# Kernel optimization log

Hardware: AMD Instinct MI355X
Metric: run time of the kernel (lower is better)

Reference implementation:

```python
import jax, jax.numpy as jnp
import numpy as np

N_NODES = 100_000
N_EDGES = 1_600_000
D = 128
BN_EPS = 1e-5
GIN_EPS = 0.0  # GINConv default eps, train_eps=False


def setup_inputs() -> dict:
    key = jax.random.key(0)
    ks = jax.random.split(key, 8)
    x = jax.random.normal(ks[0], (N_NODES, D), dtype=jnp.float32)
    edge_index = jax.random.randint(ks[1], (2, N_EDGES), 0, N_NODES, dtype=jnp.int64)
    s = 1.0 / np.sqrt(D)
    W1 = jax.random.uniform(ks[2], (D, D), jnp.float32, -s, s)
    b1 = jax.random.uniform(ks[3], (D,), jnp.float32, -s, s)
    W2 = jax.random.uniform(ks[4], (D, D), jnp.float32, -s, s)
    b2 = jax.random.uniform(ks[5], (D,), jnp.float32, -s, s)
    W3 = jax.random.uniform(ks[6], (D, D), jnp.float32, -s, s)
    g1 = jnp.ones((D,), jnp.float32)
    be1 = jnp.zeros((D,), jnp.float32)
    g2 = jnp.ones((D,), jnp.float32)
    be2 = jnp.zeros((D,), jnp.float32)
    return {"x": x, "edge_index": edge_index,
            "W1": W1, "b1": b1, "g1": g1, "be1": be1,
            "W2": W2, "b2": b2, "g2": g2, "be2": be2,
            "W3": W3}


def _batchnorm(h, gamma, beta):
    # training-mode BatchNorm1d over node dim with biased variance
    mean = jnp.mean(h, axis=0)
    var = jnp.mean(jnp.square(h - mean), axis=0)
    return (h - mean) * jax.lax.rsqrt(var + BN_EPS) * gamma + beta


def reference(x, edge_index, W1, b1, g1, be1, W2, b2, g2, be2, W3):
    src, dst = edge_index[0], edge_index[1]
    # GIN aggregation: (1+eps)*x_i + sum_{j->i} x_j  (scatter-add over edges)
    agg = jax.ops.segment_sum(x[src], dst, num_segments=N_NODES)
    h = (1.0 + GIN_EPS) * x + agg
    # MLP: Linear+BN+ReLU x2, then Linear (no bias)
    h = jax.nn.relu(_batchnorm(h @ W1.T + b1, g1, be1))
    h = jax.nn.relu(_batchnorm(h @ W2.T + b2, g2, be2))
    h = h @ W3.T
    # GINLayer final activation (bn=None)
    return jax.nn.relu(h)
```

## Files before the change

kernel.cpp:

```cpp
#include <hip/hip_runtime.h>

#define NN 100000
#define NE 1600000
#define DD 128
#define NCB 782
#define TILE 2048
#define NTILE 782
#define SREP 16
#define WPAD 17408

typedef __attribute__((ext_vector_type(8))) short bf16x8;
typedef __attribute__((ext_vector_type(4))) float f32x4;

union u4bf8 { uint4 u; bf16x8 v; };

__device__ __forceinline__ ushort f2bf(float f) {
    union { float f; uint i; } v; v.f = f;
    uint i = v.i;
    return (ushort)((i + 0x7fffu + ((i >> 16) & 1u)) >> 16);
}
__device__ __forceinline__ float bf2f(ushort u) {
    union { uint i; float f; } v; v.i = ((uint)u) << 16; return v.f;
}
__device__ __forceinline__ float blo(uint v) { return bf2f((ushort)(v & 0xffffu)); }
__device__ __forceinline__ float bhi(uint v) { return bf2f((ushort)(v >> 16)); }

__global__ __launch_bounds__(256) void k_xbh(const float* __restrict__ x,
                                             uint* __restrict__ xb,
                                             const int* __restrict__ ei,
                                             int* __restrict__ ghistP,
                                             const float* __restrict__ W1,
                                             const float* __restrict__ W2,
                                             const float* __restrict__ W3,
                                             ushort* __restrict__ Wbp) {
    __shared__ int h[NCB];
    int t = threadIdx.x;
    for (int i = t; i < NCB; i += 256) h[i] = 0;
    __syncthreads();
    int base = blockIdx.x * TILE;
#pragma unroll
    for (int i = 0; i < 8; ++i) {
        int e = base + i * 256 + t;
        if (e < NE) atomicAdd(&h[ei[NE + e] >> 7], 1);
    }
    int gid = blockIdx.x * 256 + t;
#pragma unroll
    for (int i = 0; i < 8; ++i) {
        int item = i * (NTILE * 256) + gid;
        if (item < NN * 16) {
            int n = item >> 4, q = item & 15;
            const float* xp = x + (size_t)n * DD + q * 8;
            float4 a = *(const float4*)xp;
            float4 b = *(const float4*)(xp + 4);
            uint4 pk;
            pk.x = (uint)f2bf(a.x) | ((uint)f2bf(a.y) << 16);
            pk.y = (uint)f2bf(a.z) | ((uint)f2bf(a.w) << 16);
            pk.z = (uint)f2bf(b.x) | ((uint)f2bf(b.y) << 16);
            pk.w = (uint)f2bf(b.z) | ((uint)f2bf(b.w) << 16);
            *(uint4*)(xb + (size_t)n * 64 + q * 4) = pk;
        }
    }
    int c = gid;
    if (c < 6144) {
        int l = c >> 11;
        int cc = c & 2047;
        int r = cc >> 4, c8 = (cc & 15) * 8;
        const float* Wl = (l == 0) ? W1 : (l == 1) ? W2 : W3;
        const float* p = Wl + r * DD + c8;
        float4 a = *(const float4*)p;
        float4 b = *(const float4*)(p + 4);
        uint4 pk;
        pk.x = (uint)f2bf(a.x) | ((uint)f2bf(a.y) << 16);
        pk.y = (uint)f2bf(a.z) | ((uint)f2bf(a.w) << 16);
        pk.z = (uint)f2bf(b.x) | ((uint)f2bf(b.y) << 16);
        pk.w = (uint)f2bf(b.z) | ((uint)f2bf(b.w) << 16);
        *(uint4*)&Wbp[(size_t)l * WPAD + r * 136 + c8] = pk;
    }
    __syncthreads();
    for (int i = t; i < NCB; i += 256)
        if (h[i] > 0) atomicAdd(&ghistP[i * 16], h[i]);
}

__global__ void k_cscan(const int* __restrict__ ghistP, int* __restrict__ cb,
                        int* __restrict__ gcurP) {
    __shared__ int sh[1024];
    int t = threadIdx.x;
    int my = (t < NCB) ? ghistP[t * 16] : 0;
    sh[t] = my;
    __syncthreads();
    for (int o = 1; o < 1024; o <<= 1) {
        int u = (t >= o) ? sh[t - o] : 0;
        __syncthreads();
        sh[t] += u;
        __syncthreads();
    }
    if (t < NCB) { int ex = sh[t] - my; cb[t] = ex; gcurP[t * 16] = ex; }
    if (t == NCB - 1) cb[NCB] = sh[t];
}

__global__ __launch_bounds__(256) void k_cscatter(const int* __restrict__ ei,
                                                  int* __restrict__ gcurP,
                                                  uint* __restrict__ buck) {
    __shared__ int h[NCB];
    __shared__ int tb[NCB];
    int t = threadIdx.x;
    for (int i = t; i < NCB; i += 256) h[i] = 0;
    __syncthreads();
    int base = blockIdx.x * TILE;
    uint vv[8]; int bb[8], rr[8];
#pragma unroll
    for (int i = 0; i < 8; ++i) {
        int e = base + i * 256 + t;
        bb[i] = -1;
        if (e < NE) {
            int s = ei[e], d = ei[NE + e];
            int b = d >> 7;
            bb[i] = b;
            vv[i] = (uint)s | ((uint)(d & 127) << 17);
            rr[i] = atomicAdd(&h[b], 1);
        }
    }
    __syncthreads();
    for (int i = t; i < NCB; i += 256)
        if (h[i] > 0) tb[i] = atomicAdd(&gcurP[i * 16], h[i]);
    __syncthreads();
#pragma unroll
    for (int i = 0; i < 8; ++i) {
        if (bb[i] >= 0) buck[tb[bb[i]] + rr[i]] = vv[i];
    }
}

__global__ __launch_bounds__(256) void k_fsort(const uint* __restrict__ buck,
                                               const int* __restrict__ cb,
                                               int* __restrict__ csr,
                                               int* __restrict__ rowp) {
    __shared__ int cnt[128];
    __shared__ int sd[64];
    int c = blockIdx.x, t = threadIdx.x;
    if (t < 128) cnt[t] = 0;
    __syncthreads();
    int s0 = cb[c], s1 = cb[c + 1];
    for (int i = s0 + t; i < s1; i += 256)
        atomicAdd(&cnt[(buck[i] >> 17) & 127], 1);
    __syncthreads();
    int p = 0, q = 0;
    if (t < 64) { p = cnt[2 * t]; q = cnt[2 * t + 1]; sd[t] = p + q; }
    __syncthreads();
    for (int o = 1; o < 64; o <<= 1) {
        int u = (t >= o && t < 64) ? sd[t - o] : 0;
        __syncthreads();
        if (t < 64) sd[t] += u;
        __syncthreads();
    }
    if (t < 64) {
        int base = sd[t] - (p + q);
        rowp[c * 128 + 2 * t]     = s0 + base;
        rowp[c * 128 + 2 * t + 1] = s0 + base + p;
        cnt[2 * t] = base;
        cnt[2 * t + 1] = base + p;
    }
    __syncthreads();
    for (int i = s0 + t; i < s1; i += 256) {
        uint v = buck[i];
        int ld = (int)((v >> 17) & 127u);
        int pos = atomicAdd(&cnt[ld], 1);
        csr[s0 + pos] = (int)(v & 0x1FFFFu);
    }
}

#define B8(ACC0, ACC1, SJ, J)                                               \
    {                                                                       \
        int s0 = __shfl(SJ, J),     s1 = __shfl(SJ, J + 1);                 \
        int s2 = __shfl(SJ, J + 2), s3 = __shfl(SJ, J + 3);                 \
        int s4 = __shfl(SJ, J + 4), s5 = __shfl(SJ, J + 5);                 \
        int s6 = __shfl(SJ, J + 6), s7 = __shfl(SJ, J + 7);                 \
        uint v0 = xb[(size_t)s0 * 64 + lane], v1 = xb[(size_t)s1 * 64 + lane]; \
        uint v2 = xb[(size_t)s2 * 64 + lane], v3 = xb[(size_t)s3 * 64 + lane]; \
        uint v4 = xb[(size_t)s4 * 64 + lane], v5 = xb[(size_t)s5 * 64 + lane]; \
        uint v6 = xb[(size_t)s6 * 64 + lane], v7 = xb[(size_t)s7 * 64 + lane]; \
        ACC0 += blo(v0) + blo(v1) + blo(v2) + blo(v3)                       \
              + blo(v4) + blo(v5) + blo(v6) + blo(v7);                      \
        ACC1 += bhi(v0) + bhi(v1) + bhi(v2) + bhi(v3)                       \
              + bhi(v4) + bhi(v5) + bhi(v6) + bhi(v7);                      \
    }

__global__ __launch_bounds__(256) void k_gather(const uint* __restrict__ xb,
                                                const int* __restrict__ rowp,
                                                const int* __restrict__ csr,
                                                ushort* __restrict__ agg) {
    const int HALF = NN / 2;
    int wave = threadIdx.x >> 6, lane = threadIdx.x & 63;
    int w = blockIdx.x * 4 + wave;
    if (w >= HALF) return;
    int nA = w, nB = w + HALF;
    uint sA = xb[(size_t)nA * 64 + lane];
    uint sB = xb[(size_t)nB * 64 + lane];
    float a0 = blo(sA), a1 = bhi(sA);
    float b0 = blo(sB), b1 = bhi(sB);
    int iA = rowp[nA], eA = rowp[nA + 1];
    int iB = rowp[nB], eB = rowp[nB + 1];

    while (iA < eA || iB < eB) {
        int mA = eA - iA; if (mA > 64) mA = 64; if (mA < 0) mA = 0;
        int mB = eB - iB; if (mB > 64) mB = 64; if (mB < 0) mB = 0;
        int sjA = (lane < mA) ? csr[iA + lane] : 0;
        int sjB = (lane < mB) ? csr[iB + lane] : 0;
        int j = 0, k = 0;
        while (j + 8 <= mA && k + 8 <= mB) {
            int t0 = __shfl(sjA, j),     t1 = __shfl(sjA, j + 1);
            int t2 = __shfl(sjA, j + 2), t3 = __shfl(sjA, j + 3);
            int t4 = __shfl(sjA, j + 4), t5 = __shfl(sjA, j + 5);
            int t6 = __shfl(sjA, j + 6), t7 = __shfl(sjA, j + 7);
            int u0 = __shfl(sjB, k),     u1 = __shfl(sjB, k + 1);
            int u2 = __shfl(sjB, k + 2), u3 = __shfl(sjB, k + 3);
            int u4 = __shfl(sjB, k + 4), u5 = __shfl(sjB, k + 5);
            int u6 = __shfl(sjB, k + 6), u7 = __shfl(sjB, k + 7);
            uint vA0 = xb[(size_t)t0 * 64 + lane], vA1 = xb[(size_t)t1 * 64 + lane];
            uint vA2 = xb[(size_t)t2 * 64 + lane], vA3 = xb[(size_t)t3 * 64 + lane];
            uint vA4 = xb[(size_t)t4 * 64 + lane], vA5 = xb[(size_t)t5 * 64 + lane];
            uint vA6 = xb[(size_t)t6 * 64 + lane], vA7 = xb[(size_t)t7 * 64 + lane];
            uint vB0 = xb[(size_t)u0 * 64 + lane], vB1 = xb[(size_t)u1 * 64 + lane];
            uint vB2 = xb[(size_t)u2 * 64 + lane], vB3 = xb[(size_t)u3 * 64 + lane];
            uint vB4 = xb[(size_t)u4 * 64 + lane], vB5 = xb[(size_t)u5 * 64 + lane];
            uint vB6 = xb[(size_t)u6 * 64 + lane], vB7 = xb[(size_t)u7 * 64 + lane];
            a0 += blo(vA0) + blo(vA1) + blo(vA2) + blo(vA3)
                + blo(vA4) + blo(vA5) + blo(vA6) + blo(vA7);
            a1 += bhi(vA0) + bhi(vA1) + bhi(vA2) + bhi(vA3)
                + bhi(vA4) + bhi(vA5) + bhi(vA6) + bhi(vA7);
            b0 += blo(vB0) + blo(vB1) + blo(vB2) + blo(vB3)
                + blo(vB4) + blo(vB5) + blo(vB6) + blo(vB7);
            b1 += bhi(vB0) + bhi(vB1) + bhi(vB2) + bhi(vB3)
                + bhi(vB4) + bhi(vB5) + bhi(vB6) + bhi(vB7);
            j += 8; k += 8;
        }
        while (j + 8 <= mA) { B8(a0, a1, sjA, j) j += 8; }
        while (k + 8 <= mB) { B8(b0, b1, sjB, k) k += 8; }
        while (j < mA && k < mB) {
            int t = __shfl(sjA, j); int u = __shfl(sjB, k);
            uint vA = xb[(size_t)t * 64 + lane];
            uint vB = xb[(size_t)u * 64 + lane];
            a0 += blo(vA); a1 += bhi(vA);
            b0 += blo(vB); b1 += bhi(vB);
            ++j; ++k;
        }
        while (j < mA) {
            int t = __shfl(sjA, j++);
            uint vA = xb[(size_t)t * 64 + lane];
            a0 += blo(vA); a1 += bhi(vA);
        }
        while (k < mB) {
            int u = __shfl(sjB, k++);
            uint vB = xb[(size_t)u * 64 + lane];
            b0 += blo(vB); b1 += bhi(vB);
        }
        iA += mA; iB += mB;
    }

    uint pkA = (uint)f2bf(a0) | ((uint)f2bf(a1) << 16);
    uint pkB = (uint)f2bf(b0) | ((uint)f2bf(b1) << 16);
    ((uint*)(agg + (size_t)nA * DD))[lane] = pkA;
    ((uint*)(agg + (size_t)nB * DD))[lane] = pkB;
}

template <int MODE>
__global__ __launch_bounds__(256) void k_gemm(const ushort* __restrict__ Ain,
                                              const ushort* __restrict__ Wp,
                                              const float* __restrict__ bias,
                                              const float* __restrict__ statsIn,
                                              const float* __restrict__ g,
                                              const float* __restrict__ be,
                                              void* __restrict__ Outv,
                                              float* __restrict__ statsOut) {
    __shared__ __align__(16) ushort lw[DD * 136];
    __shared__ float red[2][4][DD];
    __shared__ float lac[2 * DD];

    int tid = threadIdx.x;
#pragma unroll
    for (int it = 0; it < 8; ++it) {
        int o8 = (it * 256 + tid) * 8;
        *(uint4*)&lw[o8] = *(const uint4*)&Wp[o8];
    }
    if (tid < 128) {
        int o8 = 16384 + tid * 8;
        *(uint4*)&lw[o8] = *(const uint4*)&Wp[o8];
    }
    if constexpr (MODE != 1) {
        if (tid < DD) {
            float S = 0.f, Q = 0.f;
#pragma unroll
            for (int r = 0; r < SREP; ++r) {
                S += statsIn[(r << 8) + tid];
                Q += statsIn[(r << 8) + DD + tid];
            }
            float inv = 1.f / (float)NN;
            float mean = S * inv;
            float var = Q * inv - mean * mean;
            float a = g[tid] * rsqrtf(var + 1e-5f);
            lac[tid] = a;
            lac[DD + tid] = be[tid] - mean * a;
        }
    }
    __syncthreads();

    int wave = tid >> 6, lane = tid & 63;
    int lm = lane & 15, quad = lane >> 4;
    int row0 = blockIdx.x * 64 + wave * 16;
    int arow = row0 + lm;
    int ar = (arow < NN) ? arow : 0;

    bf16x8 afrag[4];
#pragma unroll
    for (int kb = 0; kb < 4; ++kb) {
        int k0 = kb * 32 + quad * 8;
        const ushort* ap = Ain + (size_t)ar * DD + k0;
        u4bf8 u; u.u = *(const uint4*)ap;
        if constexpr (MODE == 1) {
            afrag[kb] = u.v;
        } else {
            uint pk[4] = {u.u.x, u.u.y, u.u.z, u.u.w};
            bf16x8 af;
#pragma unroll
            for (int jj = 0; jj < 4; ++jj) {
                int k = k0 + jj * 2;
                float v0 = blo(pk[jj]);
                float v1 = bhi(pk[jj]);
                v0 = fmaxf(fmaf(v0, lac[k], lac[DD + k]), 0.f);
                v1 = fmaxf(fmaf(v1, lac[k + 1], lac[DD + k + 1]), 0.f);
                af[jj * 2]     = (short)f2bf(v0);
                af[jj * 2 + 1] = (short)f2bf(v1);
            }
            afrag[kb] = af;
        }
    }

    f32x4 acc[8];
#pragma unroll
    for (int nt = 0; nt < 8; ++nt) {
        float bv = (MODE == 3) ? 0.f : bias[nt * 16 + lm];
        acc[nt] = (f32x4){bv, bv, bv, bv};
    }

#pragma unroll
    for (int kb = 0; kb < 4; ++kb) {
#pragma unroll
        for (int nt = 0; nt < 8; ++nt) {
            bf16x8 bfrag = *(const bf16x8*)&lw[(nt * 16 + lm) * 136 + kb * 32 + quad * 8];
            acc[nt] = __builtin_amdgcn_mfma_f32_16x16x32_bf16(afrag[kb], bfrag, acc[nt], 0, 0, 0);
        }
    }

    ushort* Out16 = (ushort*)Outv;
    float* Out32 = (float*)Outv;
    float csum[8], csq[8];
#pragma unroll
    for (int nt = 0; nt < 8; ++nt) {
        int col = nt * 16 + lm;
        float s = 0.f, q = 0.f;
#pragma unroll
        for (int r = 0; r < 4; ++r) {
            int row = row0 + quad * 4 + r;
            float v = acc[nt][r];
            if (MODE == 3) v = fmaxf(v, 0.f);
            if (row < NN) {
                if constexpr (MODE == 3) Out32[(size_t)row * DD + col] = v;
                else Out16[(size_t)row * DD + col] = f2bf(v);
                s += v;
                q += v * v;
            }
        }
        csum[nt] = s; csq[nt] = q;
    }

    if constexpr (MODE != 3) {
#pragma unroll
        for (int nt = 0; nt < 8; ++nt) {
            float s = csum[nt], q = csq[nt];
            s += __shfl_down(s, 16, 64); q += __shfl_down(q, 16, 64);
            s += __shfl_down(s, 32, 64); q += __shfl_down(q, 32, 64);
            if (quad == 0) {
                red[0][wave][nt * 16 + lm] = s;
                red[1][wave][nt * 16 + lm] = q;
            }
        }
        __syncthreads();
        if (tid < DD) {
            float S = red[0][0][tid] + red[0][1][tid] + red[0][2][tid] + red[0][3][tid];
            float Q = red[1][0][tid] + red[1][1][tid] + red[1][2][tid] + red[1][3][tid];
            int rep = (blockIdx.x & (SREP - 1)) << 8;
            atomicAdd(&statsOut[rep + tid], S);
            atomicAdd(&statsOut[rep + DD + tid], Q);
        }
    }
}

extern "C" void kernel_launch(void* const* d_in, const int* in_sizes, int n_in,
                              void* d_out, int out_size, void* d_ws, size_t ws_size,
                              hipStream_t stream) {
    const float* x   = (const float*)d_in[0];
    const int* ei    = (const int*)d_in[1];
    const float* W1  = (const float*)d_in[2];
    const float* b1  = (const float*)d_in[3];
    const float* g1  = (const float*)d_in[4];
    const float* be1 = (const float*)d_in[5];
    const float* W2  = (const float*)d_in[6];
    const float* b2  = (const float*)d_in[7];
    const float* g2  = (const float*)d_in[8];
    const float* be2 = (const float*)d_in[9];
    const float* W3  = (const float*)d_in[10];

    float* stats  = (float*)d_ws;
    float* stats2 = stats + SREP * 256;
    int* ghistP   = (int*)(stats2 + SREP * 256);
    ushort* Wbp   = (ushort*)(ghistP + NCB * 16);
    int* cb       = (int*)(Wbp + 3 * WPAD);
    int* gcurP    = cb + NCB + 4;
    int* rowp     = gcurP + NCB * 16;
    uint* buck    = (uint*)(rowp + NCB * 128 + 4);
    int* csr      = (int*)(buck + NE);
    ushort* agg   = (ushort*)(((uintptr_t)(csr + NE) + 15) & ~(uintptr_t)15);
    uint* xb     = (uint*)d_out;
    ushort* t1   = (ushort*)d_out + (size_t)NN * DD;
    ushort* t2   = agg;
    float* outp  = (float*)d_out;

    int gblk = (NN + 63) / 64;
    hipMemsetAsync(stats, 0, (2 * SREP * 256) * sizeof(float) + NCB * 16 * sizeof(int), stream);
    k_xbh<<<NTILE, 256, 0, stream>>>(x, xb, ei, ghistP, W1, W2, W3, Wbp);
    k_cscan<<<1, 1024, 0, stream>>>(ghistP, cb, gcurP);
    k_cscatter<<<NTILE, 256, 0, stream>>>(ei, gcurP, buck);
    k_fsort<<<NCB, 256, 0, stream>>>(buck, cb, csr, rowp);
    k_gather<<<(NN / 2 + 3) / 4, 256, 0, stream>>>(xb, rowp, csr, agg);
    k_gemm<1><<<gblk, 256, 0, stream>>>(agg, Wbp, b1, nullptr, nullptr, nullptr, t1, stats);
    k_gemm<2><<<gblk, 256, 0, stream>>>(t1, Wbp + WPAD, b2, stats, g1, be1, t2, stats2);
    k_gemm<3><<<gblk, 256, 0, stream>>>(t2, Wbp + 2 * WPAD, nullptr, stats2, g2, be2, outp, nullptr);
}
```

Baseline: 327.2 us.

## Build CSR with per-node degree histogram, three-pass scan, and atomic edge scatter

Replaces the two-level bucket sort (coarse 128-node buckets, then a per-bucket fine sort) with a direct CSR build. Per-node degrees come from global atomics, a three-kernel prefix scan produces row pointers, and each edge is scattered with an atomic on a per-destination cursor. This drops the intermediate bucket buffer and the fine-sort pass, at the cost of many contended global atomics and an extra scan launch. Source order within each row becomes nondeterministic, which can slightly change float summation order. SREP is also doubled, which affects the statistics buffers in the unseen GEMM code.

Result: slower. 415.2 us (+26.9%).

```diff
diff --git a/kernel.cpp b/kernel.cpp
--- a/kernel.cpp
+++ b/kernel.cpp
@@ -3,11 +3,11 @@
 #define NN 100000
 #define NE 1600000
 #define DD 128
-#define NCB 782
 #define TILE 2048
 #define NTILE 782
-#define SREP 16
+#define SREP 32
 #define WPAD 17408
+#define SCB 98
 
 typedef __attribute__((ext_vector_type(8))) short bf16x8;
 typedef __attribute__((ext_vector_type(4))) float f32x4;
@@ -28,20 +28,17 @@
 __global__ __launch_bounds__(256) void k_xbh(const float* __restrict__ x,
                                              uint* __restrict__ xb,
                                              const int* __restrict__ ei,
-                                             int* __restrict__ ghistP,
+                                             int* __restrict__ deg,
                                              const float* __restrict__ W1,
                                              const float* __restrict__ W2,
                                              const float* __restrict__ W3,
                                              ushort* __restrict__ Wbp) {
-    __shared__ int h[NCB];
     int t = threadIdx.x;
-    for (int i = t; i < NCB; i += 256) h[i] = 0;
-    __syncthreads();
     int base = blockIdx.x * TILE;
 #pragma unroll
     for (int i = 0; i < 8; ++i) {
         int e = base + i * 256 + t;
-        if (e < NE) atomicAdd(&h[ei[NE + e] >> 7], 1);
+        if (e < NE) atomicAdd(&deg[ei[NE + e]], 1);
     }
     int gid = blockIdx.x * 256 + t;
 #pragma unroll
@@ -76,16 +73,15 @@
         pk.w = (uint)f2bf(b.z) | ((uint)f2bf(b.w) << 16);
         *(uint4*)&Wbp[(size_t)l * WPAD + r * 136 + c8] = pk;
     }
-    __syncthreads();
-    for (int i = t; i < NCB; i += 256)
-        if (h[i] > 0) atomicAdd(&ghistP[i * 16], h[i]);
-}
-
-__global__ void k_cscan(const int* __restrict__ ghistP, int* __restrict__ cb,
-                        int* __restrict__ gcurP) {
+}
+
+__global__ __launch_bounds__(1024) void k_scan1(const int* __restrict__ deg,
+                                                int* __restrict__ rowp,
+                                                int* __restrict__ bsum) {
     __shared__ int sh[1024];
-    int t = threadIdx.x;
-    int my = (t < NCB) ? ghistP[t * 16] : 0;
+    int t = threadIdx.x, b = blockIdx.x;
+    int n = b * 1024 + t;
+    int my = (n < NN) ? deg[n] : 0;
     sh[t] = my;
     __syncthreads();
     for (int o = 1; o < 1024; o <<= 1) {
@@ -94,77 +90,51 @@
         sh[t] += u;
         __syncthreads();
     }
-    if (t < NCB) { int ex = sh[t] - my; cb[t] = ex; gcurP[t * 16] = ex; }
-    if (t == NCB - 1) cb[NCB] = sh[t];
-}
-
-__global__ __launch_bounds__(256) void k_cscatter(const int* __restrict__ ei,
-                                                  int* __restrict__ gcurP,
-                                                  uint* __restrict__ buck) {
-    __shared__ int h[NCB];
-    __shared__ int tb[NCB];
+    if (n < NN) rowp[n] = sh[t] - my;
+    if (t == 1023) bsum[b] = sh[t];
+}
+
+__global__ void k_scan2(const int* __restrict__ bsum, int* __restrict__ boff) {
+    __shared__ int sh[128];
     int t = threadIdx.x;
-    for (int i = t; i < NCB; i += 256) h[i] = 0;
+    int my = (t < SCB) ? bsum[t] : 0;
+    sh[t] = my;
     __syncthreads();
+    for (int o = 1; o < 128; o <<= 1) {
+        int u = (t >= o) ? sh[t - o] : 0;
+        __syncthreads();
+        sh[t] += u;
+        __syncthreads();
+    }
+    if (t < SCB) boff[t] = sh[t] - my;
+}
+
+__global__ __launch_bounds__(1024) void k_scan3(int* __restrict__ rowp,
+                                                int* __restrict__ cur,
+                                                const int* __restrict__ boff) {
+    int t = threadIdx.x, b = blockIdx.x;
+    int n = b * 1024 + t;
+    if (n < NN) {
+        int v = rowp[n] + boff[b];
+        rowp[n] = v;
+        cur[n] = v;
+    }
+    if (n == 0) rowp[NN] = NE;
+}
+
+__global__ __launch_bounds__(256) void k_escatter(const int* __restrict__ ei,
+                                                  int* __restrict__ cur,
+                                                  int* __restrict__ csr) {
+    int t = threadIdx.x;
     int base = blockIdx.x * TILE;
-    uint vv[8]; int bb[8], rr[8];
 #pragma unroll
     for (int i = 0; i < 8; ++i) {
         int e = base + i * 256 + t;
-        bb[i] = -1;
         if (e < NE) {
             int s = ei[e], d = ei[NE + e];
-            int b = d >> 7;
-            bb[i] = b;
-            vv[i] = (uint)s | ((uint)(d & 127) << 17);
-            rr[i] = atomicAdd(&h[b], 1);
-        }
-    }
-    __syncthreads();
-    for (int i = t; i < NCB; i += 256)
-        if (h[i] > 0) tb[i] = atomicAdd(&gcurP[i * 16], h[i]);
-    __syncthreads();
-#pragma unroll
-    for (int i = 0; i < 8; ++i) {
-        if (bb[i] >= 0) buck[tb[bb[i]] + rr[i]] = vv[i];
-    }
-}
-
-__global__ __launch_bounds__(256) void k_fsort(const uint* __restrict__ buck,
-                                               const int* __restrict__ cb,
-                                               int* __restrict__ csr,
-                                               int* __restrict__ rowp) {
-    __shared__ int cnt[128];
-    __shared__ int sd[64];
-    int c = blockIdx.x, t = threadIdx.x;
-    if (t < 128) cnt[t] = 0;
-    __syncthreads();
-    int s0 = cb[c], s1 = cb[c + 1];
-    for (int i = s0 + t; i < s1; i += 256)
-        atomicAdd(&cnt[(buck[i] >> 17) & 127], 1);
-    __syncthreads();
-    int p = 0, q = 0;
-    if (t < 64) { p = cnt[2 * t]; q = cnt[2 * t + 1]; sd[t] = p + q; }
-    __syncthreads();
-    for (int o = 1; o < 64; o <<= 1) {
-        int u = (t >= o && t < 64) ? sd[t - o] : 0;
-        __syncthreads();
-        if (t < 64) sd[t] += u;
-        __syncthreads();
-    }
-    if (t < 64) {
-        int base = sd[t] - (p + q);
-        rowp[c * 128 + 2 * t]     = s0 + base;
-        rowp[c * 128 + 2 * t + 1] = s0 + base + p;
-        cnt[2 * t] = base;
-        cnt[2 * t + 1] = base + p;
-    }
-    __syncthreads();
-    for (int i = s0 + t; i < s1; i += 256) {
-        uint v = buck[i];
-        int ld = (int)((v >> 17) & 127u);
-        int pos = atomicAdd(&cnt[ld], 1);
-        csr[s0 + pos] = (int)(v & 0x1FFFFu);
+            int pos = atomicAdd(&cur[d], 1);
+            csr[pos] = s;
+        }
     }
 }
 
@@ -411,13 +381,13 @@
 
     float* stats  = (float*)d_ws;
     float* stats2 = stats + SREP * 256;
-    int* ghistP   = (int*)(stats2 + SREP * 256);
-    ushort* Wbp   = (ushort*)(ghistP + NCB * 16);
-    int* cb       = (int*)(Wbp + 3 * WPAD);
-    int* gcurP    = cb + NCB + 4;
-    int* rowp     = gcurP + NCB * 16;
-    uint* buck    = (uint*)(rowp + NCB * 128 + 4);
-    int* csr      = (int*)(buck + NE);
+    int* deg      = (int*)(stats2 + SREP * 256);
+    int* bsum     = deg + SCB * 1024;
+    int* boff     = bsum + 128;
+    int* rowp     = boff + 128;
+    int* cur      = rowp + NN + 4;
+    ushort* Wbp   = (ushort*)(((uintptr_t)(cur + NN) + 15) & ~(uintptr_t)15);
+    int* csr      = (int*)(((uintptr_t)(Wbp + 3 * WPAD) + 15) & ~(uintptr_t)15);
     ushort* agg   = (ushort*)(((uintptr_t)(csr + NE) + 15) & ~(uintptr_t)15);
     uint* xb     = (uint*)d_out;
     ushort* t1   = (ushort*)d_out + (size_t)NN * DD;
@@ -425,11 +395,12 @@
     float* outp  = (float*)d_out;
 
     int gblk = (NN + 63) / 64;
-    hipMemsetAsync(stats, 0, (2 * SREP * 256) * sizeof(float) + NCB * 16 * sizeof(int), stream);
-    k_xbh<<<NTILE, 256, 0, stream>>>(x, xb, ei, ghistP, W1, W2, W3, Wbp);
-    k_cscan<<<1, 1024, 0, stream>>>(ghistP, cb, gcurP);
-    k_cscatter<<<NTILE, 256, 0, stream>>>(ei, gcurP, buck);
-    k_fsort<<<NCB, 256, 0, stream>>>(buck, cb, csr, rowp);
+    hipMemsetAsync(stats, 0, (2 * SREP * 256) * sizeof(float) + SCB * 1024 * sizeof(int), stream);
+    k_xbh<<<NTILE, 256, 0, stream>>>(x, xb, ei, deg, W1, W2, W3, Wbp);
+    k_scan1<<<SCB, 1024, 0, stream>>>(deg, rowp, bsum);
+    k_scan2<<<1, 128, 0, stream>>>(bsum, boff);
+    k_scan3<<<SCB, 1024, 0, stream>>>(rowp, cur, boff);
+    k_escatter<<<NTILE, 256, 0, stream>>>(ei, cur, csr);
     k_gather<<<(NN / 2 + 3) / 4, 256, 0, stream>>>(xb, rowp, csr, agg);
     k_gemm<1><<<gblk, 256, 0, stream>>>(agg, Wbp, b1, nullptr, nullptr, nullptr, t1, stats);
     k_gemm<2><<<gblk, 256, 0, stream>>>(t1, Wbp + WPAD, b2, stats, g1, be1, t2, stats2);
```

## Coarsen CSR buckets to 512 rows and stage GEMM outputs through LDS

Applied to the files above, without the earlier changes.

The bucketed counting sort now uses 196 coarse buckets of 512 destination nodes instead of 782 buckets of 128. This cuts global atomics and makes the histogram, scan and scatter loops single-pass per thread, while each fine-sort block handles more edges. The GEMM epilogue now writes its accumulator tile into shared memory (reusing the weight buffer) and stores each output row with coalesced 16-byte vector writes, replacing scattered 2- and 4-byte stores. SREP is doubled to spread the BN-stat atomics. This adds an extra barrier and an LDS round trip per GEMM block, and fewer, larger sort blocks could reduce parallelism.

After: 313.7 us. 4.1% less time.

```diff
diff --git a/kernel.cpp b/kernel.cpp
--- a/kernel.cpp
+++ b/kernel.cpp
@@ -3,10 +3,10 @@
 #define NN 100000
 #define NE 1600000
 #define DD 128
-#define NCB 782
+#define NCB 196
 #define TILE 2048
 #define NTILE 782
-#define SREP 16
+#define SREP 32
 #define WPAD 17408
 
 typedef __attribute__((ext_vector_type(8))) short bf16x8;
@@ -35,13 +35,13 @@
                                              ushort* __restrict__ Wbp) {
     __shared__ int h[NCB];
     int t = threadIdx.x;
-    for (int i = t; i < NCB; i += 256) h[i] = 0;
+    if (t < NCB) h[t] = 0;
     __syncthreads();
     int base = blockIdx.x * TILE;
 #pragma unroll
     for (int i = 0; i < 8; ++i) {
         int e = base + i * 256 + t;
-        if (e < NE) atomicAdd(&h[ei[NE + e] >> 7], 1);
+        if (e < NE) atomicAdd(&h[ei[NE + e] >> 9], 1);
     }
     int gid = blockIdx.x * 256 + t;
 #pragma unroll
@@ -77,18 +77,17 @@
         *(uint4*)&Wbp[(size_t)l * WPAD + r * 136 + c8] = pk;
     }
     __syncthreads();
-    for (int i = t; i < NCB; i += 256)
-        if (h[i] > 0) atomicAdd(&ghistP[i * 16], h[i]);
+    if (t < NCB && h[t] > 0) atomicAdd(&ghistP[t * 16], h[t]);
 }
 
 __global__ void k_cscan(const int* __restrict__ ghistP, int* __restrict__ cb,
                         int* __restrict__ gcurP) {
-    __shared__ int sh[1024];
+    __shared__ int sh[256];
     int t = threadIdx.x;
     int my = (t < NCB) ? ghistP[t * 16] : 0;
     sh[t] = my;
     __syncthreads();
-    for (int o = 1; o < 1024; o <<= 1) {
+    for (int o = 1; o < 256; o <<= 1) {
         int u = (t >= o) ? sh[t - o] : 0;
         __syncthreads();
         sh[t] += u;
@@ -104,7 +103,7 @@
     __shared__ int h[NCB];
     __shared__ int tb[NCB];
     int t = threadIdx.x;
-    for (int i = t; i < NCB; i += 256) h[i] = 0;
+    if (t < NCB) h[t] = 0;
     __syncthreads();
     int base = blockIdx.x * TILE;
     uint vv[8]; int bb[8], rr[8];
@@ -114,15 +113,14 @@
         bb[i] = -1;
         if (e < NE) {
             int s = ei[e], d = ei[NE + e];
-            int b = d >> 7;
+            int b = d >> 9;
             bb[i] = b;
-            vv[i] = (uint)s | ((uint)(d & 127) << 17);
+            vv[i] = (uint)s | ((uint)(d & 511) << 17);
             rr[i] = atomicAdd(&h[b], 1);
         }
     }
     __syncthreads();
-    for (int i = t; i < NCB; i += 256)
-        if (h[i] > 0) tb[i] = atomicAdd(&gcurP[i * 16], h[i]);
+    if (t < NCB && h[t] > 0) tb[t] = atomicAdd(&gcurP[t * 16], h[t]);
     __syncthreads();
 #pragma unroll
     for (int i = 0; i < 8; ++i) {
@@ -134,35 +132,34 @@
                                                const int* __restrict__ cb,
                                                int* __restrict__ csr,
                                                int* __restrict__ rowp) {
-    __shared__ int cnt[128];
-    __shared__ int sd[64];
+    __shared__ int cnt[512];
+    __shared__ int sd[256];
     int c = blockIdx.x, t = threadIdx.x;
-    if (t < 128) cnt[t] = 0;
+    cnt[t] = 0; cnt[t + 256] = 0;
     __syncthreads();
     int s0 = cb[c], s1 = cb[c + 1];
     for (int i = s0 + t; i < s1; i += 256)
-        atomicAdd(&cnt[(buck[i] >> 17) & 127], 1);
-    __syncthreads();
-    int p = 0, q = 0;
-    if (t < 64) { p = cnt[2 * t]; q = cnt[2 * t + 1]; sd[t] = p + q; }
-    __syncthreads();
-    for (int o = 1; o < 64; o <<= 1) {
-        int u = (t >= o && t < 64) ? sd[t - o] : 0;
+        atomicAdd(&cnt[(buck[i] >> 17) & 511], 1);
+    __syncthreads();
+    int p = cnt[2 * t], q = cnt[2 * t + 1];
+    sd[t] = p + q;
+    __syncthreads();
+    for (int o = 1; o < 256; o <<= 1) {
+        int u = (t >= o) ? sd[t - o] : 0;
         __syncthreads();
-        if (t < 64) sd[t] += u;
+        sd[t] += u;
         __syncthreads();
     }
-    if (t < 64) {
-        int base = sd[t] - (p + q);
-        rowp[c * 128 + 2 * t]     = s0 + base;
-        rowp[c * 128 + 2 * t + 1] = s0 + base + p;
-        cnt[2 * t] = base;
-        cnt[2 * t + 1] = base + p;
-    }
+    int base = sd[t] - (p + q);
+    rowp[c * 512 + 2 * t]     = s0 + base;
+    rowp[c * 512 + 2 * t + 1] = s0 + base + p;
+    __syncthreads();
+    cnt[2 * t] = base;
+    cnt[2 * t + 1] = base + p;
     __syncthreads();
     for (int i = s0 + t; i < s1; i += 256) {
         uint v = buck[i];
-        int ld = (int)((v >> 17) & 127u);
+        int ld = (int)((v >> 17) & 511u);
         int pos = atomicAdd(&cnt[ld], 1);
         csr[s0 + pos] = (int)(v & 0x1FFFFu);
     }
@@ -271,7 +268,9 @@
                                               const float* __restrict__ be,
                                               void* __restrict__ Outv,
                                               float* __restrict__ statsOut) {
-    __shared__ __align__(16) ushort lw[DD * 136];
+    __shared__ __align__(16) char smem[DD * 136 * 2];
+    ushort* lw = (ushort*)smem;
+    float* sm32 = (float*)smem;
     __shared__ float red[2][4][DD];
     __shared__ float lac[2 * DD];
 
@@ -350,26 +349,61 @@
         }
     }
 
-    ushort* Out16 = (ushort*)Outv;
-    float* Out32 = (float*)Outv;
     float csum[8], csq[8];
+    if constexpr (MODE != 3) {
+#pragma unroll
+        for (int nt = 0; nt < 8; ++nt) {
+            float s = 0.f, q = 0.f;
+#pragma unroll
+            for (int r = 0; r < 4; ++r) {
+                int row = row0 + quad * 4 + r;
+                float v = acc[nt][r];
+                if (row < NN) { s += v; q += v * v; }
+            }
+            csum[nt] = s; csq[nt] = q;
+        }
+    }
+
+    __syncthreads();
 #pragma unroll
     for (int nt = 0; nt < 8; ++nt) {
-        int col = nt * 16 + lm;
-        float s = 0.f, q = 0.f;
 #pragma unroll
         for (int r = 0; r < 4; ++r) {
-            int row = row0 + quad * 4 + r;
+            int lrow = wave * 16 + quad * 4 + r;
             float v = acc[nt][r];
             if (MODE == 3) v = fmaxf(v, 0.f);
-            if (row < NN) {
-                if constexpr (MODE == 3) Out32[(size_t)row * DD + col] = v;
-                else Out16[(size_t)row * DD + col] = f2bf(v);
-                s += v;
-                q += v * v;
+            sm32[lrow * 132 + nt * 16 + lm] = v;
+        }
+    }
+    __syncthreads();
+
+    {
+        int row = tid >> 2, seg = tid & 3;
+        int grow = blockIdx.x * 64 + row;
+        if (grow < NN) {
+            const float* rp = sm32 + row * 132 + seg * 32;
+            if constexpr (MODE == 3) {
+                float* Out32 = (float*)Outv;
+#pragma unroll
+                for (int u = 0; u < 8; ++u) {
+                    float4 o;
+                    o.x = rp[u * 4]; o.y = rp[u * 4 + 1];
+                    o.z = rp[u * 4 + 2]; o.w = rp[u * 4 + 3];
+                    *(float4*)&Out32[(size_t)grow * DD + seg * 32 + u * 4] = o;
+                }
+            } else {
+                ushort* Out16 = (ushort*)Outv;
+#pragma unroll
+                for (int u = 0; u < 4; ++u) {
+                    uint4 pk;
+                    pk.x = (uint)f2bf(rp[u * 8])     | ((uint)f2bf(rp[u * 8 + 1]) << 16);
+                    pk.y = (uint)f2bf(rp[u * 8 + 2]) | ((uint)f2bf(rp[u * 8 + 3]) << 16);
+                    pk.z = (uint)f2bf(rp[u * 8 + 4]) | ((uint)f2bf(rp[u * 8 + 5]) << 16);
+                    pk.w = (uint)f2bf(rp[u * 8 + 6]) | ((uint)f2bf(rp[u * 8 + 7]) << 16);
+                    *(uint4*)&Out16[(size_t)grow * DD + seg * 32 + u * 8] = pk;
+                }
             }
         }
-        csum[nt] = s; csq[nt] = q;
     }
 
     if constexpr (MODE != 3) {
@@ -416,7 +450,7 @@
     int* cb       = (int*)(Wbp + 3 * WPAD);
     int* gcurP    = cb + NCB + 4;
     int* rowp     = gcurP + NCB * 16;
-    uint* buck    = (uint*)(rowp + NCB * 128 + 4);
+    uint* buck    = (uint*)(rowp + NCB * 512 + 4);
     int* csr      = (int*)(buck + NE);
     ushort* agg   = (ushort*)(((uintptr_t)(csr + NE) + 15) & ~(uintptr_t)15);
     uint* xb     = (uint*)d_out;
@@ -427,7 +461,7 @@
     int gblk = (NN + 63) / 64;
     hipMemsetAsync(stats, 0, (2 * SREP * 256) * sizeof(float) + NCB * 16 * sizeof(int), stream);
     k_xbh<<<NTILE, 256, 0, stream>>>(x, xb, ei, ghistP, W1, W2, W3, Wbp);
-    k_cscan<<<1, 1024, 0, stream>>>(ghistP, cb, gcurP);
+    k_cscan<<<1, 256, 0, stream>>>(ghistP, cb, gcurP);
     k_cscatter<<<NTILE, 256, 0, stream>>>(ei, gcurP, buck);
     k_fsort<<<NCB, 256, 0, stream>>>(buck, cb, csr, rowp);
     k_gather<<<(NN / 2 + 3) / 4, 256, 0, stream>>>(xb, rowp, csr, agg);
```
